# Optimization experiments

Hardware: AMD Instinct MI355X
Metric: run time of the kernel (lower is better)

The kernel has to match this reference:

```python
import jax, jax.numpy as jnp
import numpy as np

N_NODES = 200000
N_EDGES = 3200000
NUM_GRAPHS = 100
NODES_PER_GRAPH = 2000
D_IN = 128
D_HID = 128
D_OUT = 64


def setup_inputs() -> dict:
    key = jax.random.key(0)
    ks = jax.random.split(key, 8)
    features = jax.random.normal(ks[0], (N_NODES, D_IN), dtype=jnp.float32)
    src = jax.random.randint(ks[1], (N_EDGES,), 0, N_NODES, dtype=jnp.int32)
    dst = jax.random.randint(ks[2], (N_EDGES,), 0, N_NODES, dtype=jnp.int32)
    to_fetch = jax.random.randint(ks[3], (NUM_GRAPHS,), 0, NODES_PER_GRAPH, dtype=jnp.int32)
    w1 = jax.random.normal(ks[4], (D_IN, D_HID), dtype=jnp.float32) * (1.0 / np.sqrt(D_IN))
    b1 = jnp.zeros((D_HID,), dtype=jnp.float32)
    w2 = jax.random.normal(ks[5], (D_HID, D_HID), dtype=jnp.float32) * (1.0 / np.sqrt(D_HID))
    b2 = jnp.zeros((D_HID,), dtype=jnp.float32)
    w3 = jax.random.normal(ks[6], (D_OUT, D_HID), dtype=jnp.float32) * (1.0 / np.sqrt(D_HID))  # F.linear weight [out, in]
    b3 = jnp.zeros((D_OUT,), dtype=jnp.float32)
    return {"features": features, "src": src, "dst": dst, "to_fetch": to_fetch,
            "w1": w1, "b1": b1, "w2": w2, "b2": b2, "w3": w3, "b3": b3}


def _graph_conv(h, src, dst, norm, w, b):
    # DGL GraphConv (in_feats == out_feats branch): normalize, aggregate copy_src/sum, matmul, normalize, bias, relu
    h = h * norm
    agg = jax.ops.segment_sum(h[src], dst, num_segments=N_NODES)  # [N, d]
    rst = jnp.matmul(agg, w) * norm + b
    return jax.nn.relu(rst)


def reference(features, src, dst, to_fetch, w1, b1, w2, b2, w3, b3):
    # in-degree based symmetric-ish norm (DGL uses in_degrees for both sides here)
    deg = jax.ops.segment_sum(jnp.ones((N_EDGES,), jnp.float32), dst, num_segments=N_NODES)
    norm = jnp.power(jnp.clip(deg, 1.0), -0.5)[:, None]  # [N, 1]
    h = _graph_conv(features, src, dst, norm, w1, b1)
    h = _graph_conv(h, src, dst, norm, w2, b2)
    # fetch one node per batched graph: offsets = cumsum of batch_num_nodes
    offsets = jnp.arange(NUM_GRAPHS, dtype=jnp.int32) * NODES_PER_GRAPH
    h = h[to_fetch + offsets]  # [B, d]
    h = jnp.matmul(h, w3.T) + b3  # F.linear
    return h
```

## Files before the change

### kernel.cpp

```cpp
#include <hip/hip_runtime.h>

#define NNODES 200000
#define NEDGES 3200000
#define NGRAPH 100
#define NPG    2000
#define D      128
#define DOUT   64
#define CAP1   4096
#define CAP2   8192
#define CAPE   65536
#define FBUF   1024

__global__ void prek(int* deg, int* s1idx, unsigned char* need,
                     float* agg1, float* agg2, int* cnt) {
    int n = blockIdx.x * blockDim.x + threadIdx.x;
    if (n < NNODES) { deg[n] = 0; s1idx[n] = -1; need[n] = 0; }
    if (n < CAP1 * D) agg1[n] = 0.0f;
    if (n < NGRAPH * D) agg2[n] = 0.0f;
    if (n < 8) cnt[n] = 0;
}

__global__ void passAC(const int* __restrict__ src, const int4* __restrict__ dst4,
                       const int* __restrict__ to_fetch,
                       int* e2src, int* e2slot, int* s1idx, int* s1nodes,
                       unsigned char* need, int* cnt) {
    __shared__ int tf[NGRAPH];
    __shared__ int lcnt, lbase;
    __shared__ int bufs[FBUF], bufj[FBUF];
    int tid = threadIdx.x;
    for (int i = tid; i < NGRAPH; i += blockDim.x) tf[i] = to_fetch[i];
    if (blockIdx.x == 0 && tid < NGRAPH) need[to_fetch[tid] + tid * NPG] = 1;
    if (tid == 0) lcnt = 0;
    __syncthreads();
    const int NV = NEDGES / 4;
    int stride = gridDim.x * blockDim.x;
    for (int v = blockIdx.x * blockDim.x + tid; v < NV; v += stride) {
        int4 d4 = dst4[v];
        int ds[4] = {d4.x, d4.y, d4.z, d4.w};
        #pragma unroll
        for (int q = 0; q < 4; ++q) {
            int d = ds[q];
            int slot = d / NPG;
            if (tf[slot] == d - slot * NPG) {
                int s = src[v * 4 + q];
                int p = atomicAdd(&lcnt, 1);
                if (p < FBUF) { bufs[p] = s; bufj[p] = slot; }
                bool win = (atomicCAS(&s1idx[s], -1, -2) == -1);
                unsigned long long mask = __ballot(win ? 1 : 0);
                if (mask) {
                    int lane = tid & 63;
                    int lead = __ffsll(mask) - 1;
                    int nw = __popcll(mask);
                    int base = 0;
                    if (lane == lead) base = atomicAdd(&cnt[1], nw);
                    base = __shfl(base, lead, 64);
                    if (win) {
                        int idx = base + __popcll(mask & ((1ull << lane) - 1ull));
                        if (idx < CAP1) { s1idx[s] = idx; s1nodes[idx] = s; need[s] = 1; }
                        else s1idx[s] = -1;
                    }
                }
            }
        }
    }
    __syncthreads();
    {
        int n = min(lcnt, FBUF);
        if (tid == 0) lbase = atomicAdd(&cnt[0], n);
        __syncthreads();
        for (int k = tid; k < n; k += blockDim.x) {
            int g = lbase + k;
            if (g < CAP2) { e2src[g] = bufs[k]; e2slot[g] = bufj[k]; }
        }
    }
}

__global__ void passB(const int* __restrict__ src, const int4* __restrict__ dst4,
                      const int* __restrict__ s1idx, unsigned char* need,
                      int* e1src, int* e1j, int* cnt) {
    __shared__ int lcnt, lbase;
    __shared__ int bufs[FBUF], bufj[FBUF];
    int tid = threadIdx.x;
    if (tid == 0) lcnt = 0;
    __syncthreads();
    const int NV = NEDGES / 4;
    int stride = gridDim.x * blockDim.x;
    for (int v = blockIdx.x * blockDim.x + tid; v < NV; v += stride) {
        int4 d4 = dst4[v];
        int ds[4] = {d4.x, d4.y, d4.z, d4.w};
        #pragma unroll
        for (int q = 0; q < 4; ++q) {
            int j = s1idx[ds[q]];
            if (j >= 0) {
                int s = src[v * 4 + q];
                need[s] = 1;
                int p = atomicAdd(&lcnt, 1);
                if (p < FBUF) { bufs[p] = s; bufj[p] = j; }
            }
        }
    }
    __syncthreads();
    {
        int n = min(lcnt, FBUF);
        if (tid == 0) lbase = atomicAdd(&cnt[2], n);
        __syncthreads();
        for (int k = tid; k < n; k += blockDim.x) {
            int g = lbase + k;
            if (g < CAPE) { e1src[g] = bufs[k]; e1j[g] = bufj[k]; }
        }
    }
}

__global__ void passC(const int4* __restrict__ dst4, const unsigned char* __restrict__ need,
                      int* deg) {
    const int NV = NEDGES / 4;
    int stride = gridDim.x * blockDim.x;
    for (int v = blockIdx.x * blockDim.x + threadIdx.x; v < NV; v += stride) {
        int4 d4 = dst4[v];
        int ds[4] = {d4.x, d4.y, d4.z, d4.w};
        #pragma unroll
        for (int q = 0; q < 4; ++q)
            if (need[ds[q]]) atomicAdd(&deg[ds[q]], 1);
    }
}

__global__ void agg1_kernel(const int* __restrict__ e1src, const int* __restrict__ e1j,
                            const int* __restrict__ cnt, const int* __restrict__ deg,
                            const float* __restrict__ feat, float* agg1) {
    int t = threadIdx.x;
    int ne = min(cnt[2], CAPE);
    for (int e = blockIdx.x; e < ne; e += gridDim.x) {
        int s = e1src[e];
        float nm = rsqrtf(fmaxf((float)deg[s], 1.0f));
        float v = feat[(size_t)s * D + t] * nm;
        atomicAdd(&agg1[e1j[e] * D + t], v);
    }
}

__global__ void gemm1(const float* __restrict__ agg1, const float* __restrict__ w1,
                      const float* __restrict__ b1, const int* __restrict__ deg,
                      const int* __restrict__ s1nodes, const int* __restrict__ cnt,
                      float* h1n) {
    int nj = min(cnt[1], CAP1);
    int t = threadIdx.x;
    __shared__ float sa[D];
    for (int j = blockIdx.x; j < nj; j += gridDim.x) {
        __syncthreads();
        sa[t] = agg1[j * D + t];
        __syncthreads();
        float acc = 0.0f;
        #pragma unroll
        for (int k = 0; k < D; k++) acc += sa[k] * w1[k * D + t];
        float nm = rsqrtf(fmaxf((float)deg[s1nodes[j]], 1.0f));
        h1n[j * D + t] = fmaxf(acc * nm + b1[t], 0.0f) * nm;
    }
}

__global__ void agg2_kernel(const int* __restrict__ e2src, const int* __restrict__ e2slot,
                            const int* __restrict__ s1idx, const int* __restrict__ cnt,
                            const float* __restrict__ h1n, float* agg2) {
    int t = threadIdx.x;
    int ne = min(cnt[0], CAP2);
    for (int e = blockIdx.x; e < ne; e += gridDim.x) {
        int j = s1idx[e2src[e]];
        if (j >= 0) atomicAdd(&agg2[e2slot[e] * D + t], h1n[j * D + t]);
    }
}

__global__ void final_kernel(const float* __restrict__ agg2, const float* __restrict__ w2,
                             const float* __restrict__ b2, const int* __restrict__ deg,
                             const int* __restrict__ to_fetch,
                             const float* __restrict__ w3, const float* __restrict__ b3,
                             float* out) {
    int i = blockIdx.x;
    int t = threadIdx.x;
    __shared__ float sa[D], h2[D];
    sa[t] = agg2[i * D + t];
    __syncthreads();
    float acc = 0.0f;
    #pragma unroll
    for (int k = 0; k < D; k++) acc += sa[k] * w2[k * D + t];
    float nm = rsqrtf(fmaxf((float)deg[to_fetch[i] + i * NPG], 1.0f));
    h2[t] = fmaxf(acc * nm + b2[t], 0.0f);
    __syncthreads();
    if (t < DOUT) {
        float o = 0.0f;
        #pragma unroll
        for (int k = 0; k < D; k++) o += h2[k] * w3[t * D + k];
        out[i * DOUT + t] = o + b3[t];
    }
}

extern "C" void kernel_launch(void* const* d_in, const int* in_sizes, int n_in,
                              void* d_out, int out_size, void* d_ws, size_t ws_size,
                              hipStream_t stream) {
    const float* feat     = (const float*)d_in[0];
    const int*   src      = (const int*)  d_in[1];
    const int*   dst      = (const int*)  d_in[2];
    const int*   to_fetch = (const int*)  d_in[3];
    const float* w1       = (const float*)d_in[4];
    const float* b1       = (const float*)d_in[5];
    const float* w2       = (const float*)d_in[6];
    const float* b2       = (const float*)d_in[7];
    const float* w3       = (const float*)d_in[8];
    const float* b3       = (const float*)d_in[9];
    float* out = (float*)d_out;
    const int4* dst4 = (const int4*)dst;

    char* p = (char*)d_ws;
    int*   deg     = (int*)p;            p += (size_t)NNODES * 4;
    int*   s1idx   = (int*)p;            p += (size_t)NNODES * 4;
    int*   s1nodes = (int*)p;            p += (size_t)CAP1 * 4;
    int*   e2src   = (int*)p;            p += (size_t)CAP2 * 4;
    int*   e2slot  = (int*)p;            p += (size_t)CAP2 * 4;
    int*   e1src   = (int*)p;            p += (size_t)CAPE * 4;
    int*   e1j     = (int*)p;            p += (size_t)CAPE * 4;
    float* agg1    = (float*)p;          p += (size_t)CAP1 * D * 4;
    float* h1n     = (float*)p;          p += (size_t)CAP1 * D * 4;
    float* agg2    = (float*)p;          p += (size_t)NGRAPH * D * 4;
    int*   cnt     = (int*)p;            p += 64;
    unsigned char* need = (unsigned char*)p; p += (size_t)NNODES;

    prek<<<(CAP1 * D + 255) / 256, 256, 0, stream>>>(deg, s1idx, need, agg1, agg2, cnt);
    passAC<<<2048, 256, 0, stream>>>(src, dst4, to_fetch, e2src, e2slot,
                                     s1idx, s1nodes, need, cnt);
    passB<<<2048, 256, 0, stream>>>(src, dst4, s1idx, need, e1src, e1j, cnt);
    passC<<<2048, 256, 0, stream>>>(dst4, need, deg);
    agg1_kernel<<<2048, 128, 0, stream>>>(e1src, e1j, cnt, deg, feat, agg1);
    gemm1<<<CAP1, 128, 0, stream>>>(agg1, w1, b1, deg, s1nodes, cnt, h1n);
    agg2_kernel<<<1024, 128, 0, stream>>>(e2src, e2slot, s1idx, cnt, h1n, agg2);
    final_kernel<<<NGRAPH, 128, 0, stream>>>(agg2, w2, b2, deg, to_fetch, w3, b3, out);
}
```

Baseline: 149.3 us.

## Fuse edge-scan passes and agg1 into one persistent kernel with grid barriers

Merges passAC, passB, passC and agg1 into a single persistent kernel of 768 blocks that separates the phases with a software grid barrier built from spread-out atomic counters. The aim is to remove three kernel launch boundaries and their drain and refill gaps between the full edge scans. Cross-phase writes now use relaxed agent-scope atomic stores so other blocks see them after the barrier. The scheme assumes all 768 blocks are resident at once, otherwise the barrier deadlocks. It also runs fewer blocks per scan than the previous 2048-block launches.

```diff
diff --git a/kernel.cpp b/kernel.cpp
--- a/kernel.cpp
+++ b/kernel.cpp
@@ -10,31 +10,68 @@
 #define CAP2   8192
 #define CAPE   65536
 #define FBUF   1024
+#define NBLK   768
+#define BLINES 8
+
+__device__ __forceinline__ void stg(int* p, int v) {
+    __hip_atomic_store(p, v, __ATOMIC_RELAXED, __HIP_MEMORY_SCOPE_AGENT);
+}
+__device__ __forceinline__ void stg8(unsigned char* p, unsigned char v) {
+    __hip_atomic_store(p, v, __ATOMIC_RELAXED, __HIP_MEMORY_SCOPE_AGENT);
+}
+__device__ __forceinline__ int ldga(const int* p) {
+    return __hip_atomic_load((int*)p, __ATOMIC_RELAXED, __HIP_MEMORY_SCOPE_AGENT);
+}
 
 __global__ void prek(int* deg, int* s1idx, unsigned char* need,
-                     float* agg1, float* agg2, int* cnt) {
+                     float* agg1, float* agg2, int* cnt, int* bar) {
     int n = blockIdx.x * blockDim.x + threadIdx.x;
     if (n < NNODES) { deg[n] = 0; s1idx[n] = -1; need[n] = 0; }
     if (n < CAP1 * D) agg1[n] = 0.0f;
     if (n < NGRAPH * D) agg2[n] = 0.0f;
     if (n < 8) cnt[n] = 0;
-}
-
-__global__ void passAC(const int* __restrict__ src, const int4* __restrict__ dst4,
-                       const int* __restrict__ to_fetch,
-                       int* e2src, int* e2slot, int* s1idx, int* s1nodes,
-                       unsigned char* need, int* cnt) {
+    if (n < 3 * BLINES * 16) bar[n] = 0;
+}
+
+__device__ __forceinline__ void gridbar(int* bar, int bi) {
+    __syncthreads();
+    if (threadIdx.x == 0) {
+        asm volatile("s_waitcnt vmcnt(0) lgkmcnt(0)" ::: "memory");
+        atomicAdd(&bar[bi * BLINES * 16 + (blockIdx.x & (BLINES - 1)) * 16], 1);
+        int s;
+        do {
+            s = 0;
+            #pragma unroll
+            for (int i = 0; i < BLINES; i++)
+                s += __hip_atomic_load(&bar[bi * BLINES * 16 + i * 16],
+                                       __ATOMIC_RELAXED, __HIP_MEMORY_SCOPE_AGENT);
+            if (s < NBLK) __builtin_amdgcn_s_sleep(2);
+        } while (s < NBLK);
+    }
+    __syncthreads();
+    asm volatile("" ::: "memory");
+}
+
+__global__ __launch_bounds__(256, 4) void megascan(
+        const int* __restrict__ src, const int4* __restrict__ dst4,
+        const int* __restrict__ to_fetch, const float* __restrict__ feat,
+        int* e2src, int* e2slot, int* s1idx, int* s1nodes, unsigned char* need,
+        int* e1src, int* e1j, int* deg, float* agg1, int* cnt, int* bar) {
+
+    const int tid = threadIdx.x;
+    const int bid = blockIdx.x;
+    const int NV = NEDGES / 4;
+    const int stride = NBLK * 256;
+
     __shared__ int tf[NGRAPH];
     __shared__ int lcnt, lbase;
     __shared__ int bufs[FBUF], bufj[FBUF];
-    int tid = threadIdx.x;
-    for (int i = tid; i < NGRAPH; i += blockDim.x) tf[i] = to_fetch[i];
-    if (blockIdx.x == 0 && tid < NGRAPH) need[to_fetch[tid] + tid * NPG] = 1;
+
+    for (int i = tid; i < NGRAPH; i += 256) tf[i] = to_fetch[i];
     if (tid == 0) lcnt = 0;
     __syncthreads();
-    const int NV = NEDGES / 4;
-    int stride = gridDim.x * blockDim.x;
-    for (int v = blockIdx.x * blockDim.x + tid; v < NV; v += stride) {
+    if (bid == 0 && tid < NGRAPH) stg8(&need[tf[tid] + tid * NPG], 1);
+    for (int v = bid * 256 + tid; v < NV; v += stride) {
         int4 d4 = dst4[v];
         int ds[4] = {d4.x, d4.y, d4.z, d4.w};
         #pragma unroll
@@ -56,8 +93,11 @@
                     base = __shfl(base, lead, 64);
                     if (win) {
                         int idx = base + __popcll(mask & ((1ull << lane) - 1ull));
-                        if (idx < CAP1) { s1idx[s] = idx; s1nodes[idx] = s; need[s] = 1; }
-                        else s1idx[s] = -1;
+                        if (idx < CAP1) {
+                            stg(&s1idx[s], idx);
+                            s1nodes[idx] = s;
+                            stg8(&need[s], 1);
+                        } else stg(&s1idx[s], -1);
                     }
                 }
             }
@@ -68,24 +108,16 @@
         int n = min(lcnt, FBUF);
         if (tid == 0) lbase = atomicAdd(&cnt[0], n);
         __syncthreads();
-        for (int k = tid; k < n; k += blockDim.x) {
+        for (int k = tid; k < n; k += 256) {
             int g = lbase + k;
             if (g < CAP2) { e2src[g] = bufs[k]; e2slot[g] = bufj[k]; }
         }
-    }
-}
-
-__global__ void passB(const int* __restrict__ src, const int4* __restrict__ dst4,
-                      const int* __restrict__ s1idx, unsigned char* need,
-                      int* e1src, int* e1j, int* cnt) {
-    __shared__ int lcnt, lbase;
-    __shared__ int bufs[FBUF], bufj[FBUF];
-    int tid = threadIdx.x;
-    if (tid == 0) lcnt = 0;
-    __syncthreads();
-    const int NV = NEDGES / 4;
-    int stride = gridDim.x * blockDim.x;
-    for (int v = blockIdx.x * blockDim.x + tid; v < NV; v += stride) {
+        __syncthreads();
+        if (tid == 0) lcnt = 0;
+    }
+    gridbar(bar, 0);
+
+    for (int v = bid * 256 + tid; v < NV; v += stride) {
         int4 d4 = dst4[v];
         int ds[4] = {d4.x, d4.y, d4.z, d4.w};
         #pragma unroll
@@ -93,7 +125,7 @@
             int j = s1idx[ds[q]];
             if (j >= 0) {
                 int s = src[v * 4 + q];
-                need[s] = 1;
+                stg8(&need[s], 1);
                 int p = atomicAdd(&lcnt, 1);
                 if (p < FBUF) { bufs[p] = s; bufj[p] = j; }
             }
@@ -104,36 +136,32 @@
         int n = min(lcnt, FBUF);
         if (tid == 0) lbase = atomicAdd(&cnt[2], n);
         __syncthreads();
-        for (int k = tid; k < n; k += blockDim.x) {
+        for (int k = tid; k < n; k += 256) {
             int g = lbase + k;
-            if (g < CAPE) { e1src[g] = bufs[k]; e1j[g] = bufj[k]; }
-        }
-    }
-}
-
-__global__ void passC(const int4* __restrict__ dst4, const unsigned char* __restrict__ need,
-                      int* deg) {
-    const int NV = NEDGES / 4;
-    int stride = gridDim.x * blockDim.x;
-    for (int v = blockIdx.x * blockDim.x + threadIdx.x; v < NV; v += stride) {
+            if (g < CAPE) { stg(&e1src[g], bufs[k]); stg(&e1j[g], bufj[k]); }
+        }
+    }
+    gridbar(bar, 1);
+
+    for (int v = bid * 256 + tid; v < NV; v += stride) {
         int4 d4 = dst4[v];
         int ds[4] = {d4.x, d4.y, d4.z, d4.w};
         #pragma unroll
         for (int q = 0; q < 4; ++q)
             if (need[ds[q]]) atomicAdd(&deg[ds[q]], 1);
     }
-}
-
-__global__ void agg1_kernel(const int* __restrict__ e1src, const int* __restrict__ e1j,
-                            const int* __restrict__ cnt, const int* __restrict__ deg,
-                            const float* __restrict__ feat, float* agg1) {
-    int t = threadIdx.x;
-    int ne = min(cnt[2], CAPE);
-    for (int e = blockIdx.x; e < ne; e += gridDim.x) {
-        int s = e1src[e];
-        float nm = rsqrtf(fmaxf((float)deg[s], 1.0f));
-        float v = feat[(size_t)s * D + t] * nm;
-        atomicAdd(&agg1[e1j[e] * D + t], v);
+    gridbar(bar, 2);
+
+    {
+        int ne = min(ldga(&cnt[2]), CAPE);
+        int col = tid & 127, sub = tid >> 7;
+        for (int e = bid * 2 + sub; e < ne; e += NBLK * 2) {
+            int s = e1src[e];
+            int j = e1j[e];
+            float nm = rsqrtf(fmaxf((float)deg[s], 1.0f));
+            float v = feat[(size_t)s * D + col] * nm;
+            atomicAdd(&agg1[j * D + col], v);
+        }
     }
 }
 
@@ -219,14 +247,13 @@
     float* h1n     = (float*)p;          p += (size_t)CAP1 * D * 4;
     float* agg2    = (float*)p;          p += (size_t)NGRAPH * D * 4;
     int*   cnt     = (int*)p;            p += 64;
+    int*   bar     = (int*)p;            p += 3 * BLINES * 16 * 4;
     unsigned char* need = (unsigned char*)p; p += (size_t)NNODES;
 
-    prek<<<(CAP1 * D + 255) / 256, 256, 0, stream>>>(deg, s1idx, need, agg1, agg2, cnt);
-    passAC<<<2048, 256, 0, stream>>>(src, dst4, to_fetch, e2src, e2slot,
-                                     s1idx, s1nodes, need, cnt);
-    passB<<<2048, 256, 0, stream>>>(src, dst4, s1idx, need, e1src, e1j, cnt);
-    passC<<<2048, 256, 0, stream>>>(dst4, need, deg);
-    agg1_kernel<<<2048, 128, 0, stream>>>(e1src, e1j, cnt, deg, feat, agg1);
+    prek<<<(CAP1 * D + 255) / 256, 256, 0, stream>>>(deg, s1idx, need, agg1, agg2, cnt, bar);
+    megascan<<<NBLK, 256, 0, stream>>>(src, dst4, to_fetch, feat,
+                                       e2src, e2slot, s1idx, s1nodes, need,
+                                       e1src, e1j, deg, agg1, cnt, bar);
     gemm1<<<CAP1, 128, 0, stream>>>(agg1, w1, b1, deg, s1nodes, cnt, h1n);
     agg2_kernel<<<1024, 128, 0, stream>>>(e2src, e2slot, s1idx, cnt, h1n, agg2);
     final_kernel<<<NGRAPH, 128, 0, stream>>>(agg2, w2, b2, deg, to_fetch, w3, b3, out);
```

Result: slower. 224.5 us (+50.3%).

## Replace per-node flag arrays with bitmaps cached in shared memory for edge scans

Applied to the files above, without the earlier changes.

Node membership flags (layer-1 set and needed set) become 25 KB bitmaps built with atomicOr. The passB and passC edge scans load them into LDS, so the per-edge random lookups into 800 KB/200 KB global arrays become shared-memory bit tests. Launch shapes change to 512-thread blocks, FBUF shrinks to fit LDS, and agg1 processes two edges per block. This adds atomicOr traffic and a per-block bitmap load, and the smaller FBUF raises the risk of buffer overflow truncating edges.

```diff
diff --git a/kernel.cpp b/kernel.cpp
--- a/kernel.cpp
+++ b/kernel.cpp
@@ -9,29 +9,35 @@
 #define CAP1   4096
 #define CAP2   8192
 #define CAPE   65536
-#define FBUF   1024
-
-__global__ void prek(int* deg, int* s1idx, unsigned char* need,
+#define FBUF   512
+#define BMW    6250
+
+__global__ void prek(int* deg, int* s1idx, int* s1bits, int* needbits,
                      float* agg1, float* agg2, int* cnt) {
     int n = blockIdx.x * blockDim.x + threadIdx.x;
-    if (n < NNODES) { deg[n] = 0; s1idx[n] = -1; need[n] = 0; }
+    if (n < NNODES) { deg[n] = 0; s1idx[n] = -1; }
     if (n < CAP1 * D) agg1[n] = 0.0f;
     if (n < NGRAPH * D) agg2[n] = 0.0f;
+    if (n < BMW) { s1bits[n] = 0; needbits[n] = 0; }
     if (n < 8) cnt[n] = 0;
 }
 
-__global__ void passAC(const int* __restrict__ src, const int4* __restrict__ dst4,
-                       const int* __restrict__ to_fetch,
-                       int* e2src, int* e2slot, int* s1idx, int* s1nodes,
-                       unsigned char* need, int* cnt) {
+__global__ __launch_bounds__(256) void passA(
+        const int* __restrict__ src, const int4* __restrict__ dst4,
+        const int* __restrict__ to_fetch,
+        int* e2src, int* e2slot, int* s1idx, int* s1nodes,
+        int* s1bits, int* needbits, int* cnt) {
     __shared__ int tf[NGRAPH];
     __shared__ int lcnt, lbase;
     __shared__ int bufs[FBUF], bufj[FBUF];
     int tid = threadIdx.x;
     for (int i = tid; i < NGRAPH; i += blockDim.x) tf[i] = to_fetch[i];
-    if (blockIdx.x == 0 && tid < NGRAPH) need[to_fetch[tid] + tid * NPG] = 1;
     if (tid == 0) lcnt = 0;
     __syncthreads();
+    if (blockIdx.x == 0 && tid < NGRAPH) {
+        int n2 = tf[tid] + tid * NPG;
+        atomicOr(&needbits[n2 >> 5], 1 << (n2 & 31));
+    }
     const int NV = NEDGES / 4;
     int stride = gridDim.x * blockDim.x;
     for (int v = blockIdx.x * blockDim.x + tid; v < NV; v += stride) {
@@ -56,8 +62,11 @@
                     base = __shfl(base, lead, 64);
                     if (win) {
                         int idx = base + __popcll(mask & ((1ull << lane) - 1ull));
-                        if (idx < CAP1) { s1idx[s] = idx; s1nodes[idx] = s; need[s] = 1; }
-                        else s1idx[s] = -1;
+                        if (idx < CAP1) {
+                            s1idx[s] = idx; s1nodes[idx] = s;
+                            atomicOr(&s1bits[s >> 5], 1 << (s & 31));
+                            atomicOr(&needbits[s >> 5], 1 << (s & 31));
+                        } else s1idx[s] = -1;
                     }
                 }
             }
@@ -75,12 +84,15 @@
     }
 }
 
-__global__ void passB(const int* __restrict__ src, const int4* __restrict__ dst4,
-                      const int* __restrict__ s1idx, unsigned char* need,
-                      int* e1src, int* e1j, int* cnt) {
+__global__ __launch_bounds__(512) void passB(
+        const int* __restrict__ src, const int4* __restrict__ dst4,
+        const int* __restrict__ s1bits, const int* __restrict__ s1idx,
+        int* needbits, int* e1src, int* e1j, int* cnt) {
+    __shared__ int bm[BMW];
     __shared__ int lcnt, lbase;
     __shared__ int bufs[FBUF], bufj[FBUF];
     int tid = threadIdx.x;
+    for (int i = tid; i < BMW; i += blockDim.x) bm[i] = s1bits[i];
     if (tid == 0) lcnt = 0;
     __syncthreads();
     const int NV = NEDGES / 4;
@@ -90,10 +102,11 @@
         int ds[4] = {d4.x, d4.y, d4.z, d4.w};
         #pragma unroll
         for (int q = 0; q < 4; ++q) {
-            int j = s1idx[ds[q]];
-            if (j >= 0) {
+            int d = ds[q];
+            if (bm[d >> 5] & (1 << (d & 31))) {
+                int j = s1idx[d];
                 int s = src[v * 4 + q];
-                need[s] = 1;
+                atomicOr(&needbits[s >> 5], 1 << (s & 31));
                 int p = atomicAdd(&lcnt, 1);
                 if (p < FBUF) { bufs[p] = s; bufj[p] = j; }
             }
@@ -111,29 +124,35 @@
     }
 }
 
-__global__ void passC(const int4* __restrict__ dst4, const unsigned char* __restrict__ need,
-                      int* deg) {
+__global__ __launch_bounds__(512) void passC(
+        const int4* __restrict__ dst4, const int* __restrict__ needbits, int* deg) {
+    __shared__ int bm[BMW];
+    int tid = threadIdx.x;
+    for (int i = tid; i < BMW; i += blockDim.x) bm[i] = needbits[i];
+    __syncthreads();
     const int NV = NEDGES / 4;
     int stride = gridDim.x * blockDim.x;
-    for (int v = blockIdx.x * blockDim.x + threadIdx.x; v < NV; v += stride) {
+    for (int v = blockIdx.x * blockDim.x + tid; v < NV; v += stride) {
         int4 d4 = dst4[v];
         int ds[4] = {d4.x, d4.y, d4.z, d4.w};
         #pragma unroll
-        for (int q = 0; q < 4; ++q)
-            if (need[ds[q]]) atomicAdd(&deg[ds[q]], 1);
+        for (int q = 0; q < 4; ++q) {
+            int d = ds[q];
+            if (bm[d >> 5] & (1 << (d & 31))) atomicAdd(&deg[d], 1);
+        }
     }
 }
 
 __global__ void agg1_kernel(const int* __restrict__ e1src, const int* __restrict__ e1j,
                             const int* __restrict__ cnt, const int* __restrict__ deg,
                             const float* __restrict__ feat, float* agg1) {
-    int t = threadIdx.x;
+    int col = threadIdx.x & 127, sub = threadIdx.x >> 7;
     int ne = min(cnt[2], CAPE);
-    for (int e = blockIdx.x; e < ne; e += gridDim.x) {
+    for (int e = blockIdx.x * 2 + sub; e < ne; e += gridDim.x * 2) {
         int s = e1src[e];
         float nm = rsqrtf(fmaxf((float)deg[s], 1.0f));
-        float v = feat[(size_t)s * D + t] * nm;
-        atomicAdd(&agg1[e1j[e] * D + t], v);
+        float v = feat[(size_t)s * D + col] * nm;
+        atomicAdd(&agg1[e1j[e] * D + col], v);
     }
 }
 
@@ -208,25 +227,28 @@
     const int4* dst4 = (const int4*)dst;
 
     char* p = (char*)d_ws;
-    int*   deg     = (int*)p;            p += (size_t)NNODES * 4;
-    int*   s1idx   = (int*)p;            p += (size_t)NNODES * 4;
-    int*   s1nodes = (int*)p;            p += (size_t)CAP1 * 4;
-    int*   e2src   = (int*)p;            p += (size_t)CAP2 * 4;
-    int*   e2slot  = (int*)p;            p += (size_t)CAP2 * 4;
-    int*   e1src   = (int*)p;            p += (size_t)CAPE * 4;
-    int*   e1j     = (int*)p;            p += (size_t)CAPE * 4;
-    float* agg1    = (float*)p;          p += (size_t)CAP1 * D * 4;
-    float* h1n     = (float*)p;          p += (size_t)CAP1 * D * 4;
-    float* agg2    = (float*)p;          p += (size_t)NGRAPH * D * 4;
-    int*   cnt     = (int*)p;            p += 64;
-    unsigned char* need = (unsigned char*)p; p += (size_t)NNODES;
-
-    prek<<<(CAP1 * D + 255) / 256, 256, 0, stream>>>(deg, s1idx, need, agg1, agg2, cnt);
-    passAC<<<2048, 256, 0, stream>>>(src, dst4, to_fetch, e2src, e2slot,
-                                     s1idx, s1nodes, need, cnt);
-    passB<<<2048, 256, 0, stream>>>(src, dst4, s1idx, need, e1src, e1j, cnt);
-    passC<<<2048, 256, 0, stream>>>(dst4, need, deg);
-    agg1_kernel<<<2048, 128, 0, stream>>>(e1src, e1j, cnt, deg, feat, agg1);
+    int*   deg      = (int*)p;           p += (size_t)NNODES * 4;
+    int*   s1idx    = (int*)p;           p += (size_t)NNODES * 4;
+    int*   s1nodes  = (int*)p;           p += (size_t)CAP1 * 4;
+    int*   e2src    = (int*)p;           p += (size_t)CAP2 * 4;
+    int*   e2slot   = (int*)p;           p += (size_t)CAP2 * 4;
+    int*   e1src    = (int*)p;           p += (size_t)CAPE * 4;
+    int*   e1j      = (int*)p;           p += (size_t)CAPE * 4;
+    float* agg1     = (float*)p;         p += (size_t)CAP1 * D * 4;
+    float* h1n      = (float*)p;         p += (size_t)CAP1 * D * 4;
+    float* agg2     = (float*)p;         p += (size_t)NGRAPH * D * 4;
+    int*   s1bits   = (int*)p;           p += (size_t)BMW * 4;
+    int*   needbits = (int*)p;           p += (size_t)BMW * 4;
+    int*   cnt      = (int*)p;           p += 64;
+
+    prek<<<(CAP1 * D + 255) / 256, 256, 0, stream>>>(deg, s1idx, s1bits, needbits,
+                                                     agg1, agg2, cnt);
+    passA<<<2048, 256, 0, stream>>>(src, dst4, to_fetch, e2src, e2slot,
+                                    s1idx, s1nodes, s1bits, needbits, cnt);
+    passB<<<1024, 512, 0, stream>>>(src, dst4, s1bits, s1idx, needbits,
+                                    e1src, e1j, cnt);
+    passC<<<1024, 512, 0, stream>>>(dst4, needbits, deg);
+    agg1_kernel<<<2048, 256, 0, stream>>>(e1src, e1j, cnt, deg, feat, agg1);
     gemm1<<<CAP1, 128, 0, stream>>>(agg1, w1, b1, deg, s1nodes, cnt, h1n);
     agg2_kernel<<<1024, 128, 0, stream>>>(e2src, e2slot, s1idx, cnt, h1n, agg2);
     final_kernel<<<NGRAPH, 128, 0, stream>>>(agg2, w2, b2, deg, to_fetch, w3, b3, out);
```

Result: faster. 133.8 us (-10.4%).
